# Kernel optimization log

Measured on AMD Instinct MI355X. Metric: run time of the kernel, lower is better.

The kernel has to match this reference:

```python
import jax, jax.numpy as jnp
import numpy as np

B = 100000      # query points
L = 8           # num levels
N_RBF = 256     # RBF centers per level
F = 16          # features per level
OUT = 3         # output dim


def setup_inputs() -> dict:
    key = jax.random.key(0)
    k = jax.random.split(key, 6)
    x = jax.random.normal(k[0], (B, 3), dtype=jnp.float32)
    # small-magnitude features so gaussian RBF responses are non-degenerate
    feats = 0.1 * jax.random.normal(k[1], (B, L * F), dtype=jnp.float32)
    # centers initialized uniform(-1e-4, 1e-4) as in the torch module
    centers = jax.random.uniform(k[2], (L, N_RBF, F), dtype=jnp.float32,
                                 minval=-1e-4, maxval=1e-4)
    # log-width parameters (exp'd in forward); small perturbation around 0
    betas = 0.01 * jax.random.normal(k[3], (L, N_RBF, F), dtype=jnp.float32)
    W = jax.random.normal(k[4], (OUT, N_RBF * L), dtype=jnp.float32) / np.sqrt(N_RBF * L)
    b = jax.random.normal(k[5], (OUT,), dtype=jnp.float32) * 0.01
    return {"x": x, "feats": feats, "centers": centers, "betas": betas, "W": W, "b": b}


def reference(x, feats, centers, betas, W, b):
    # centers, betas: [L, N, F]. x is unused by the original forward (faithful).
    Lnum, N, f = centers.shape
    rbfs = []
    for i in range(Lnum):
        # concat of first i+1 per-level tables along feature axis -> [N, (i+1)*f]
        C = centers[: i + 1].transpose(1, 0, 2).reshape(N, (i + 1) * f)
        Bw = jnp.exp(betas[: i + 1].transpose(1, 0, 2).reshape(N, (i + 1) * f))
        x_in = feats[:, : (i + 1) * f]                      # [B, (i+1)*f]
        term1 = (x_in * x_in) @ Bw.T                        # [B, N]
        term2 = x_in @ (Bw * C).T                           # [B, N]
        term3 = jnp.sum(Bw * C * C, axis=1)                 # [N]
        dist_sq = term1 - 2.0 * term2 + term3[None, :]
        rbfs.append(jnp.exp(-0.5 * dist_sq))                # gaussian basis
    outs = jnp.concatenate(rbfs, axis=-1)                   # [B, L*N]
    return outs @ W.T + b
```

## Files before the change

### kernel.cpp

```cpp
#include <hip/hip_runtime.h>
#include <math.h>

#define LN 8
#define NRBF 256
#define FD 16
#define OUTD 3
#define KC (-0.72134752044f)

typedef __attribute__((ext_vector_type(8))) short short8;
typedef __attribute__((ext_vector_type(4))) float floatx4;

__device__ __forceinline__ short f2bf(float f) {
    unsigned u = __builtin_bit_cast(unsigned, f);
    u += 0x7fffu + ((u >> 16) & 1u);
    return (short)(u >> 16);
}


__global__ __launch_bounds__(256) void prep(
    const float* __restrict__ centers, const float* __restrict__ betas,
    const float* __restrict__ W, short* __restrict__ PKB, float* __restrict__ EPI)
{
    __shared__ float ls[LN * 32];
    int blk = blockIdx.x;
    int tid = threadIdx.x;
    if (blk < 32) {
        int t = blk * 256 + tid;
        int lane = t & 63;
        int nt   = (t >> 6) & 15;
        int j    = t >> 10;
        int n    = nt * 16 + (lane & 15);
        int kq   = lane >> 4;
        size_t base = ((size_t)(j * NRBF + n)) * FD + kq * 4;
        float4 bq = *(const float4*)(betas + base);
        float4 cq = *(const float4*)(centers + base);
        float a0 = __expf(bq.x), a1 = __expf(bq.y), a2 = __expf(bq.z), a3 = __expf(bq.w);
        short8 v;
        v[0] = f2bf(a0); v[1] = f2bf(-2.0f * a0 * cq.x);
        v[2] = f2bf(a1); v[3] = f2bf(-2.0f * a1 * cq.y);
        v[4] = f2bf(a2); v[5] = f2bf(-2.0f * a2 * cq.z);
        v[6] = f2bf(a3); v[7] = f2bf(-2.0f * a3 * cq.w);
        *((short8*)(PKB + (size_t)t * 8)) = v;
    } else {
        int jj = tid >> 5;
        int nl = tid & 31;
        int n  = (blk - 32) * 32 + nl;
        const float* bp = betas   + ((size_t)(jj * NRBF + n)) * FD;
        const float* cp = centers + ((size_t)(jj * NRBF + n)) * FD;
        float s = 0.f;
#pragma unroll
        for (int q = 0; q < 4; ++q) {
            float4 bq = *(const float4*)(bp + q * 4);
            float4 cq = *(const float4*)(cp + q * 4);
            s = fmaf(__expf(bq.x) * cq.x, cq.x, s);
            s = fmaf(__expf(bq.y) * cq.y, cq.y, s);
            s = fmaf(__expf(bq.z) * cq.z, cq.z, s);
            s = fmaf(__expf(bq.w) * cq.w, cq.w, s);
        }
        ls[jj * 32 + nl] = s;
        __syncthreads();
        float t3 = 0.f;
        for (int j2 = 0; j2 <= jj; ++j2) t3 += ls[j2 * 32 + nl];
        float4 e;
        e.x = KC * t3;
        e.y = W[0 * (LN * NRBF) + jj * NRBF + n];
        e.z = W[1 * (LN * NRBF) + jj * NRBF + n];
        e.w = W[2 * (LN * NRBF) + jj * NRBF + n];
        int nt = n >> 4, l = n & 15;
        ((float4*)EPI)[nt * 128 + jj * 16 + l] = e;
    }
}

__global__ __launch_bounds__(256, 5) void rbf_mfma(
    const float* __restrict__ feats, const short* __restrict__ PKB,
    const float* __restrict__ EPI, const float* __restrict__ bias,
    float* __restrict__ out, int B)
{
    __shared__ short8 pk_s[2][LN * 64];
    __shared__ float4 ep_s[2][128];

    int tid  = threadIdx.x;
    int lane = tid & 63;
    int wid  = tid >> 6;
    int ntile_total = (B + 15) >> 4;
    int tile = blockIdx.x * 4 + wid;
    bool tvalid = (tile < ntile_total);
    if (!tvalid) tile = ntile_total - 1;
    int b0 = tile * 16;
    int m  = lane & 15;
    int kq = lane >> 4;

    int brow = b0 + m; if (brow >= B) brow = B - 1;
    const float* xrow = feats + (size_t)brow * (LN * FD) + kq * 4;
    short8 afrag[LN];
#pragma unroll
    for (int j = 0; j < LN; ++j) {
        float4 x = *((const float4*)(xrow + j * FD));
        short8 f;
        f[0] = f2bf(x.x * x.x); f[1] = f2bf(x.x);
        f[2] = f2bf(x.y * x.y); f[3] = f2bf(x.y);
        f[4] = f2bf(x.z * x.z); f[5] = f2bf(x.z);
        f[6] = f2bf(x.w * x.w); f[7] = f2bf(x.w);
        afrag[j] = f;
    }

    int j0 = wid * 2, j1 = wid * 2 + 1;

#define STAGE(buf, nt)                                                                  \
    do {                                                                                \
        const short* g0 = PKB + (size_t)(((j0 * 16 + (nt)) * 64 + lane)) * 8;           \
        const short* g1 = PKB + (size_t)(((j1 * 16 + (nt)) * 64 + lane)) * 8;           \
        __builtin_amdgcn_global_load_lds(                                               \
            (const __attribute__((address_space(1))) void*)g0,                          \
            (__attribute__((address_space(3))) void*)&pk_s[buf][j0 * 64], 16, 0, 0);    \
        __builtin_amdgcn_global_load_lds(                                               \
            (const __attribute__((address_space(1))) void*)g1,                          \
            (__attribute__((address_space(3))) void*)&pk_s[buf][j1 * 64], 16, 0, 0);    \
        if (wid < 2) {                                                                  \
            const float* ge = EPI + (size_t)((nt) * 128 + wid * 64 + lane) * 4;         \
            __builtin_amdgcn_global_load_lds(                                           \
                (const __attribute__((address_space(1))) void*)ge,                      \
                (__attribute__((address_space(3))) void*)&ep_s[buf][wid * 64], 16, 0, 0);\
        }                                                                               \
    } while (0)

    STAGE(0, 0);

    float oacc[12];
#pragma unroll
    for (int i = 0; i < 12; ++i) oacc[i] = 0.f;

    __syncthreads();

#pragma unroll 1
    for (int nt = 0; nt < 16; ++nt) {
        int cur = nt & 1;
        if (nt < 15) STAGE(cur ^ 1, nt + 1);
        floatx4 acc = {0.f, 0.f, 0.f, 0.f};
#pragma unroll
        for (int j = 0; j < LN; ++j) {
            short8 bfrag = pk_s[cur][j * 64 + lane];
            acc = __builtin_amdgcn_mfma_f32_16x16x32_bf16(afrag[j], bfrag, acc, 0, 0, 0);
            float4 e = ep_s[cur][j * 16 + m];
#pragma unroll
            for (int r = 0; r < 4; ++r) {
                float rv = __builtin_amdgcn_exp2f(fmaf(acc[r], KC, e.x));
                oacc[r * 3 + 0] = fmaf(rv, e.y, oacc[r * 3 + 0]);
                oacc[r * 3 + 1] = fmaf(rv, e.z, oacc[r * 3 + 1]);
                oacc[r * 3 + 2] = fmaf(rv, e.w, oacc[r * 3 + 2]);
            }
        }
        __syncthreads();
    }

#pragma unroll
    for (int i = 0; i < 12; ++i) {
        oacc[i] += __shfl_xor(oacc[i], 1);
        oacc[i] += __shfl_xor(oacc[i], 2);
        oacc[i] += __shfl_xor(oacc[i], 4);
        oacc[i] += __shfl_xor(oacc[i], 8);
    }

    if (tvalid && m < OUTD) {
        float bv = bias[m];
#pragma unroll
        for (int r = 0; r < 4; ++r) {
            int row = b0 + kq * 4 + r;
            float v = (m == 0) ? oacc[r * 3 + 0] : (m == 1) ? oacc[r * 3 + 1] : oacc[r * 3 + 2];
            if (row < B) out[(size_t)row * OUTD + m] = v + bv;
        }
    }
}

extern "C" void kernel_launch(void* const* d_in, const int* in_sizes, int n_in,
                              void* d_out, int out_size, void* d_ws, size_t ws_size,
                              hipStream_t stream) {
    const float* feats   = (const float*)d_in[1];
    const float* centers = (const float*)d_in[2];
    const float* betas   = (const float*)d_in[3];
    const float* W       = (const float*)d_in[4];
    const float* bias    = (const float*)d_in[5];
    float* out = (float*)d_out;
    int B = in_sizes[1] / (LN * FD);

    short* PKB = (short*)d_ws;
    float* EPI = (float*)((char*)d_ws + 65536 * 2);

    prep<<<40, 256, 0, stream>>>(centers, betas, W, PKB, EPI);

    int tiles  = (B + 15) / 16;
    int blocks = (tiles + 3) / 4;
    rbf_mfma<<<blocks, 256, 0, stream>>>(feats, PKB, EPI, bias, out, B);
}
```

Before: 167.5 us.

## Split RBF centers across waves per tile and reduce partial outputs in LDS

Each block now handles one 16-row tile, and its four waves each cover a quarter of the RBF center tiles. The double-buffered LDS staging of B fragments and epilogue constants is replaced by direct global loads, which should hit in cache. Partial outputs are combined across waves through a small LDS reduction. The epilogue accumulation now uses packed float2 FMAs. This launches four times as many blocks and requires each block to load its feature rows four times (once per wave), along with a barrier and extra LDS traffic at the end.

```diff
diff --git a/kernel.cpp b/kernel.cpp
--- a/kernel.cpp
+++ b/kernel.cpp
@@ -9,6 +9,7 @@
 
 typedef __attribute__((ext_vector_type(8))) short short8;
 typedef __attribute__((ext_vector_type(4))) float floatx4;
+typedef __attribute__((ext_vector_type(2))) float floatx2;
 
 __device__ __forceinline__ short f2bf(float f) {
     unsigned u = __builtin_bit_cast(unsigned, f);
@@ -76,19 +77,14 @@
     const float* __restrict__ EPI, const float* __restrict__ bias,
     float* __restrict__ out, int B)
 {
-    __shared__ short8 pk_s[2][LN * 64];
-    __shared__ float4 ep_s[2][128];
+    __shared__ float red[4][48];
 
     int tid  = threadIdx.x;
     int lane = tid & 63;
-    int wid  = tid >> 6;
-    int ntile_total = (B + 15) >> 4;
-    int tile = blockIdx.x * 4 + wid;
-    bool tvalid = (tile < ntile_total);
-    if (!tvalid) tile = ntile_total - 1;
-    int b0 = tile * 16;
-    int m  = lane & 15;
-    int kq = lane >> 4;
+    int w    = tid >> 6;
+    int b0   = blockIdx.x * 16;
+    int m    = lane & 15;
+    int kq   = lane >> 4;
 
     int brow = b0 + m; if (brow >= B) brow = B - 1;
     const float* xrow = feats + (size_t)brow * (LN * FD) + kq * 4;
@@ -104,55 +100,40 @@
         afrag[j] = f;
     }
 
-    int j0 = wid * 2, j1 = wid * 2 + 1;
+    floatx2 o01[4];
+    float   o2[4];
+#pragma unroll
+    for (int r = 0; r < 4; ++r) { o01[r] = (floatx2){0.f, 0.f}; o2[r] = 0.f; }
 
-#define STAGE(buf, nt)                                                                  \
-    do {                                                                                \
-        const short* g0 = PKB + (size_t)(((j0 * 16 + (nt)) * 64 + lane)) * 8;           \
-        const short* g1 = PKB + (size_t)(((j1 * 16 + (nt)) * 64 + lane)) * 8;           \
-        __builtin_amdgcn_global_load_lds(                                               \
-            (const __attribute__((address_space(1))) void*)g0,                          \
-            (__attribute__((address_space(3))) void*)&pk_s[buf][j0 * 64], 16, 0, 0);    \
-        __builtin_amdgcn_global_load_lds(                                               \
-            (const __attribute__((address_space(1))) void*)g1,                          \
-            (__attribute__((address_space(3))) void*)&pk_s[buf][j1 * 64], 16, 0, 0);    \
-        if (wid < 2) {                                                                  \
-            const float* ge = EPI + (size_t)((nt) * 128 + wid * 64 + lane) * 4;         \
-            __builtin_amdgcn_global_load_lds(                                           \
-                (const __attribute__((address_space(1))) void*)ge,                      \
-                (__attribute__((address_space(3))) void*)&ep_s[buf][wid * 64], 16, 0, 0);\
-        }                                                                               \
-    } while (0)
-
-    STAGE(0, 0);
+#pragma unroll 1
+    for (int g = 0; g < 4; ++g) {
+        int nt = w * 4 + g;
+        const short8* pb = (const short8*)PKB + (size_t)nt * 64 + lane;
+        const float4* ep = (const float4*)EPI + (size_t)nt * 128 + m;
+        floatx4 acc = {0.f, 0.f, 0.f, 0.f};
+#pragma unroll
+        for (int j = 0; j < LN; ++j) {
+            short8 bfrag = pb[j * 16 * 64];
+            float4 e     = ep[j * 16];
+            acc = __builtin_amdgcn_mfma_f32_16x16x32_bf16(afrag[j], bfrag, acc, 0, 0, 0);
+            floatx2 eyz = {e.y, e.z};
+#pragma unroll
+            for (int r = 0; r < 4; ++r) {
+                float rv = __builtin_amdgcn_exp2f(fmaf(acc[r], KC, e.x));
+                floatx2 rv2 = {rv, rv};
+                o01[r] += rv2 * eyz;
+                o2[r]   = fmaf(rv, e.w, o2[r]);
+            }
+        }
+    }
 
     float oacc[12];
 #pragma unroll
-    for (int i = 0; i < 12; ++i) oacc[i] = 0.f;
-
-    __syncthreads();
-
-#pragma unroll 1
-    for (int nt = 0; nt < 16; ++nt) {
-        int cur = nt & 1;
-        if (nt < 15) STAGE(cur ^ 1, nt + 1);
-        floatx4 acc = {0.f, 0.f, 0.f, 0.f};
-#pragma unroll
-        for (int j = 0; j < LN; ++j) {
-            short8 bfrag = pk_s[cur][j * 64 + lane];
-            acc = __builtin_amdgcn_mfma_f32_16x16x32_bf16(afrag[j], bfrag, acc, 0, 0, 0);
-            float4 e = ep_s[cur][j * 16 + m];
-#pragma unroll
-            for (int r = 0; r < 4; ++r) {
-                float rv = __builtin_amdgcn_exp2f(fmaf(acc[r], KC, e.x));
-                oacc[r * 3 + 0] = fmaf(rv, e.y, oacc[r * 3 + 0]);
-                oacc[r * 3 + 1] = fmaf(rv, e.z, oacc[r * 3 + 1]);
-                oacc[r * 3 + 2] = fmaf(rv, e.w, oacc[r * 3 + 2]);
-            }
-        }
-        __syncthreads();
+    for (int r = 0; r < 4; ++r) {
+        oacc[r * 3 + 0] = o01[r].x;
+        oacc[r * 3 + 1] = o01[r].y;
+        oacc[r * 3 + 2] = o2[r];
     }
-
 #pragma unroll
     for (int i = 0; i < 12; ++i) {
         oacc[i] += __shfl_xor(oacc[i], 1);
@@ -161,13 +142,19 @@
         oacc[i] += __shfl_xor(oacc[i], 8);
     }
 
-    if (tvalid && m < OUTD) {
-        float bv = bias[m];
+    if (m < OUTD) {
 #pragma unroll
-        for (int r = 0; r < 4; ++r) {
-            int row = b0 + kq * 4 + r;
-            float v = (m == 0) ? oacc[r * 3 + 0] : (m == 1) ? oacc[r * 3 + 1] : oacc[r * 3 + 2];
-            if (row < B) out[(size_t)row * OUTD + m] = v + bv;
+        for (int r = 0; r < 4; ++r)
+            red[w][kq * 12 + r * 3 + m] = oacc[r * 3 + m];
+    }
+    __syncthreads();
+
+    if (tid < 48) {
+        int o = tid % 3;
+        int row = b0 + tid / 3;
+        if (row < B) {
+            float s = red[0][tid] + red[1][tid] + red[2][tid] + red[3][tid] + bias[o];
+            out[(size_t)b0 * 3 + tid] = s;
         }
     }
 }
@@ -188,7 +175,6 @@
 
     prep<<<40, 256, 0, stream>>>(centers, betas, W, PKB, EPI);
 
-    int tiles  = (B + 15) / 16;
-    int blocks = (tiles + 3) / 4;
-    rbf_mfma<<<blocks, 256, 0, stream>>>(feats, PKB, EPI, bias, out, B);
+    int tiles = (B + 15) / 16;
+    rbf_mfma<<<tiles, 256, 0, stream>>>(feats, PKB, EPI, bias, out, B);
 }
```

Result: no change. 165.1 us (-1.4%).
